# Optimization experiments

Hardware: AMD Instinct MI355X
Metric: run time of the kernel (lower is better)

The kernel has to match this reference:

```python
import jax, jax.numpy as jnp
import numpy as np

DIM_HEAD = 64
LN_EPS = 1e-6  # flax nn.LayerNorm default


def setup_inputs() -> dict:
    key = jax.random.key(0)
    ks = jax.random.split(key, 5)
    B, N, D, H, Dh = 4, 1024, 768, 12, 64
    x = jax.random.normal(ks[0], (B, N, D), dtype=jnp.float32)
    Wq = jax.random.normal(ks[1], (D, H, Dh), dtype=jnp.float32) * (1.0 / np.sqrt(D))
    Wk = jax.random.normal(ks[2], (D, H, Dh), dtype=jnp.float32) * (1.0 / np.sqrt(D))
    Wv = jax.random.normal(ks[3], (D, H, Dh), dtype=jnp.float32) * (1.0 / np.sqrt(D))
    theta = jax.random.normal(ks[4], (H, H), dtype=jnp.float32) * (1.0 / np.sqrt(H))
    ln_scale = jnp.ones((N,), dtype=jnp.float32)
    ln_bias = jnp.zeros((N,), dtype=jnp.float32)
    return {"x": x, "Wq": Wq, "Wk": Wk, "Wv": Wv, "theta": theta,
            "ln_scale": ln_scale, "ln_bias": ln_bias}


def reference(x, Wq, Wk, Wv, theta, ln_scale, ln_bias):
    # x: [B, N, D]; W*: [D, H, Dh]; theta: [H, H]; ln_*: [N]
    q = jnp.einsum('bnd,dhe->bnhe', x, Wq) / jnp.sqrt(jnp.float32(DIM_HEAD))
    k = jnp.einsum('bnd,dhe->bnhe', x, Wk)
    v = jnp.einsum('bnd,dhe->bnhe', x, Wv)
    # attention scores over key axis: [B, H, N, N]
    attn = jnp.einsum('bqhd,bkhd->bhqk', q, k)
    attn = jax.nn.softmax(attn, axis=-1)
    # cross-head theta mixing: 'h i, b h q k -> b i q k'
    attn = jnp.einsum('hi,bhqk->biqk', theta, attn)
    # LayerNorm over last (key) axis with learnable scale/bias of shape [N]
    mean = jnp.mean(attn, axis=-1, keepdims=True)
    var = jnp.mean(jnp.square(attn - mean), axis=-1, keepdims=True)
    attn = (attn - mean) * jax.lax.rsqrt(var + LN_EPS) * ln_scale + ln_bias
    # note: output indexed by k (as in the original source einsum)
    out = jnp.einsum('bhqk,bqhd->bkhd', attn, v)
    B, N, H, Dh = out.shape
    return out.reshape(B, N, H * Dh)
```

## Files before the change

kernel.cpp:

```cpp
#include <hip/hip_runtime.h>

#define NB    4
#define NSEQ  1024
#define DMODEL 768
#define NH    12
#define DH    64

typedef __bf16 bf16x8 __attribute__((ext_vector_type(8)));
typedef float  floatx4 __attribute__((ext_vector_type(4)));
typedef unsigned int u32;

static __device__ __forceinline__ float bf2f(unsigned short u) {
    return __uint_as_float(((unsigned)u) << 16);
}
static __device__ __forceinline__ unsigned short f2bf(float f) {
    unsigned u = __float_as_uint(f);
    u += 0x7FFFu + ((u >> 16) & 1u);
    return (unsigned short)(u >> 16);
}

static __device__ __forceinline__ void gl_lds16(const void* g, void* l) {
    __builtin_amdgcn_global_load_lds(
        (const __attribute__((address_space(1))) unsigned int*)g,
        (__attribute__((address_space(3))) unsigned int*)l, 16, 0, 0);
}

__global__ __launch_bounds__(256) void cast_x(
    const float* __restrict__ x, unsigned short* __restrict__ xb)
{
    const int g = blockIdx.x * 256 + threadIdx.x;
    const size_t base = (size_t)g * 8;
    float4 a = *(const float4*)(x + base);
    float4 b = *(const float4*)(x + base + 4);
    unsigned short o[8];
    o[0] = f2bf(a.x); o[1] = f2bf(a.y); o[2] = f2bf(a.z); o[3] = f2bf(a.w);
    o[4] = f2bf(b.x); o[5] = f2bf(b.y); o[6] = f2bf(b.z); o[7] = f2bf(b.w);
    *(uint4*)(xb + base) = *(uint4*)o;
}

__global__ __launch_bounds__(256) void tr_w(
    const float* __restrict__ Wq, const float* __restrict__ Wk,
    const float* __restrict__ Wv, unsigned short* __restrict__ Wt)
{
    const int z  = blockIdx.z;
    const float* __restrict__ W = (z == 0) ? Wq : (z == 1) ? Wk : Wv;
    const int c0 = blockIdx.x * 64;
    const int k0 = blockIdx.y * 64;
    const int t  = threadIdx.x;

    __shared__ float ls[64][65];

    const int lr = t >> 2;
    #pragma unroll
    for (int j = 0; j < 4; j++) {
        int col = (t & 3) * 16 + j * 4;
        float4 v = *(const float4*)(W + (size_t)(k0 + lr) * DMODEL + c0 + col);
        ls[lr][col + 0] = v.x; ls[lr][col + 1] = v.y;
        ls[lr][col + 2] = v.z; ls[lr][col + 3] = v.w;
    }
    __syncthreads();
    const int lc = t >> 2;
    #pragma unroll
    for (int j = 0; j < 4; j++) {
        int kb = (t & 3) * 16 + j * 4;
        ushort4 o;
        o.x = f2bf(ls[kb + 0][lc]); o.y = f2bf(ls[kb + 1][lc]);
        o.z = f2bf(ls[kb + 2][lc]); o.w = f2bf(ls[kb + 3][lc]);
        *(ushort4*)(Wt + (size_t)z * DMODEL * DMODEL + (size_t)(c0 + lc) * DMODEL + k0 + kb) = o;
    }
}

__global__ __launch_bounds__(256) void qkv_mfma(
    const unsigned short* __restrict__ xb, const unsigned short* __restrict__ Wt,
    unsigned short* __restrict__ Q, unsigned short* __restrict__ K,
    unsigned short* __restrict__ V)
{
    const int z  = blockIdx.z;
    const int r0 = blockIdx.x * 64;
    const int c0 = blockIdx.y * 128;
    const int t    = threadIdx.x;
    const int wave = t >> 6, lane = t & 63;
    const int m = lane & 15, g = lane >> 4;

    const unsigned short* __restrict__ B = Wt + (size_t)z * DMODEL * DMODEL;

    __shared__ __align__(16) char sm[17408];
    unsigned short (*As)[32] = (unsigned short(*)[32])sm;
    unsigned short (*Bs)[32] = (unsigned short(*)[32])(sm + 4096);
    unsigned short (*Po)[136] = (unsigned short(*)[136])sm;

    const int wm = (wave >> 1) * 32;
    const int wn = (wave & 1) * 64;

    floatx4 acc[2][4] = {};

    const unsigned short* ga  = xb + (size_t)(r0 + (t >> 2)) * DMODEL + (t & 3) * 8;
    const unsigned short* gb0 = B  + (size_t)(c0 + (t >> 2)) * DMODEL + (t & 3) * 8;
    const unsigned short* gb1 = B  + (size_t)(c0 + 64 + (t >> 2)) * DMODEL + (t & 3) * 8;
    unsigned short* la  = (unsigned short*)sm + (size_t)t * 8;
    unsigned short* lb0 = (unsigned short*)(sm + 4096) + (size_t)t * 8;
    unsigned short* lb1 = (unsigned short*)(sm + 4096) + (size_t)(t + 256) * 8;

    for (int kk = 0; kk < DMODEL / 32; kk++) {
        gl_lds16(ga  + kk * 32, la);
        gl_lds16(gb0 + kk * 32, lb0);
        gl_lds16(gb1 + kk * 32, lb1);
        __syncthreads();

        bf16x8 af[2], bf[4];
        #pragma unroll
        for (int mt = 0; mt < 2; mt++)
            af[mt] = *(const bf16x8*)&As[wm + mt * 16 + m][g * 8];
        #pragma unroll
        for (int nt = 0; nt < 4; nt++)
            bf[nt] = *(const bf16x8*)&Bs[wn + nt * 16 + m][g * 8];
        #pragma unroll
        for (int mt = 0; mt < 2; mt++)
            #pragma unroll
            for (int nt = 0; nt < 4; nt++)
                acc[mt][nt] = __builtin_amdgcn_mfma_f32_16x16x32_bf16(
                    af[mt], bf[nt], acc[mt][nt], 0, 0, 0);
        __syncthreads();
    }

    const float scale = (z == 0) ? 0.125f : 1.0f;
    #pragma unroll
    for (int mt = 0; mt < 2; mt++) {
        #pragma unroll
        for (int nt = 0; nt < 4; nt++) {
            int rloc = wm + mt * 16 + g * 4;
            int cloc = wn + nt * 16 + m;
            #pragma unroll
            for (int r = 0; r < 4; r++)
                Po[rloc + r][cloc] = f2bf(acc[mt][nt][r] * scale);
        }
    }
    __syncthreads();

    #pragma unroll
    for (int i = 0; i < 4; i++) {
        int ci = t + i * 256;
        int row = ci >> 4, off = (ci & 15) * 8;
        uint4 val = *(uint4*)&Po[row][off];
        if (z == 0) {
            *(uint4*)(Q + (size_t)(r0 + row) * DMODEL + c0 + off) = val;
        } else {
            unsigned short* P = (z == 1) ? K : V;
            int rr = r0 + row;
            int b = rr >> 10, n = rr & 1023;
            int cc = c0 + off;
            int h = cc >> 6, d = cc & 63;
            *(uint4*)(P + (((size_t)b * NH + h) * NSEQ + n) * DH + d) = val;
        }
    }
}

__global__ __launch_bounds__(256) void score_gemm(
    const unsigned short* __restrict__ Q, const unsigned short* __restrict__ K,
    unsigned short* __restrict__ P, float* __restrict__ Lpart)
{
    const int bh = blockIdx.z;
    const int b  = bh / NH, h = bh % NH;
    const int q0 = blockIdx.x * 128;
    const int k0 = blockIdx.y * 128;
    const int t    = threadIdx.x;
    const int wave = t >> 6, lane = t & 63;

    __shared__ __align__(16) char sm[36864];
    unsigned short (*Qs)[72] = (unsigned short(*)[72])sm;
    unsigned short (*Ks)[72] = (unsigned short(*)[72])(sm + 18432);
    unsigned short (*Po)[136] = (unsigned short(*)[136])sm;
    float (*rsum)[2] = (float(*)[2])(sm + 34816);

    #pragma unroll
    for (int i = 0; i < 4; i++) {
        int c = t + i * 256;
        int row = c >> 3, off = (c & 7) * 8;
        uint4 qa = *(const uint4*)(Q + ((size_t)(b * NSEQ + q0 + row)) * DMODEL + h * DH + off);
        uint4 ka = *(const uint4*)(K + (((size_t)bh) * NSEQ + (k0 + row)) * DH + off);
        *(uint4*)&Qs[row][off] = qa;
        *(uint4*)&Ks[row][off] = ka;
    }
    __syncthreads();

    const int wq = (wave >> 1) * 64, wk2 = (wave & 1) * 64;
    const int m = lane & 15, g = lane >> 4;

    floatx4 acc[4][4] = {};
    #pragma unroll
    for (int ds = 0; ds < 2; ds++) {
        const int dd = ds * 32 + g * 8;
        bf16x8 af[4], bf[4];
        #pragma unroll
        for (int mt = 0; mt < 4; mt++)
            af[mt] = *(const bf16x8*)&Qs[wq + mt * 16 + m][dd];
        #pragma unroll
        for (int nt = 0; nt < 4; nt++)
            bf[nt] = *(const bf16x8*)&Ks[wk2 + nt * 16 + m][dd];
        #pragma unroll
        for (int mt = 0; mt < 4; mt++)
            #pragma unroll
            for (int nt = 0; nt < 4; nt++)
                acc[mt][nt] = __builtin_amdgcn_mfma_f32_16x16x32_bf16(
                    af[mt], bf[nt], acc[mt][nt], 0, 0, 0);
    }

    __syncthreads();
    float rs[4][4] = {};
    #pragma unroll
    for (int mt = 0; mt < 4; mt++) {
        #pragma unroll
        for (int nt = 0; nt < 4; nt++) {
            int qloc = wq + mt * 16 + g * 4;
            int kloc = wk2 + nt * 16 + m;
            #pragma unroll
            for (int r = 0; r < 4; r++) {
                float e = __expf(acc[mt][nt][r]);
                Po[qloc + r][kloc] = f2bf(e);
                rs[mt][r] += e;
            }
        }
    }
    #pragma unroll
    for (int mt = 0; mt < 4; mt++)
        #pragma unroll
        for (int r = 0; r < 4; r++) {
            float x = rs[mt][r];
            #pragma unroll
            for (int off = 1; off < 16; off <<= 1)
                x += __shfl_xor(x, off, 64);
            rs[mt][r] = x;
        }
    if (m == 0) {
        #pragma unroll
        for (int mt = 0; mt < 4; mt++)
            #pragma unroll
            for (int r = 0; r < 4; r++)
                rsum[wq + mt * 16 + g * 4 + r][wk2 >> 6] = rs[mt][r];
    }
    __syncthreads();

    if (t < 128)
        Lpart[((size_t)bh * 8 + blockIdx.y) * NSEQ + q0 + t] = rsum[t][0] + rsum[t][1];

    #pragma unroll
    for (int i = 0; i < 8; i++) {
        int c = t + i * 256;
        int row = c >> 4, off = (c & 15) * 8;
        *(uint4*)(P + (((size_t)bh * NSEQ) + q0 + row) * NSEQ + k0 + off) =
            *(uint4*)&Po[row][off];
    }
}

static __device__ __forceinline__ void reduce12(
    const float* v, float* out12, float* red, int t)
{
    const int lane = t & 63, w = t >> 6;
    #pragma unroll
    for (int h = 0; h < 12; h++) {
        float x = v[h];
        #pragma unroll
        for (int off = 32; off > 0; off >>= 1)
            x += __shfl_down(x, off, 64);
        if (lane == 0) red[w * 12 + h] = x;
    }
    __syncthreads();
    if (t < 12) {
        float x = red[t];
        #pragma unroll
        for (int w2 = 1; w2 < 4; w2++) x += red[w2 * 12 + t];
        out12[t] = x;
    }
    __syncthreads();
}

__global__ __launch_bounds__(256) void mix_fused(
    unsigned short* __restrict__ P, const float* __restrict__ theta,
    const float* __restrict__ Lpart,
    const float* __restrict__ ln_scale, const float* __restrict__ ln_bias)
{
    const int q = blockIdx.x, b = blockIdx.y, t = threadIdx.x;
    __shared__ float th_s[144], red[48], l_s2[12], l_mean[12], l_rstd[12];

    if (t < 12) {
        float s = 0.f;
        #pragma unroll
        for (int kt = 0; kt < 8; kt++)
            s += Lpart[(((size_t)(b * NH + t)) * 8 + kt) * NSEQ + q];
        red[36 + t] = s;
        float mean = 0.f;
        #pragma unroll
        for (int h = 0; h < 12; h++) mean += theta[h * 12 + t];
        l_mean[t] = mean * (1.0f / 1024.0f);
    }
    __syncthreads();
    if (t < 144) th_s[t] = theta[t] * (1.0f / red[36 + t / 12]);
    __syncthreads();

    unsigned short* Pq = P + ((size_t)b * NH * NSEQ + q) * NSEQ;
    const int k0 = 4 * t;

    float p[12][4];
    #pragma unroll
    for (int h = 0; h < NH; h++) {
        ushort4 u = *(const ushort4*)(Pq + (size_t)h * NSEQ * NSEQ + k0);
        p[h][0] = bf2f(u.x); p[h][1] = bf2f(u.y);
        p[h][2] = bf2f(u.z); p[h][3] = bf2f(u.w);
    }

    float sT2[12];
    #pragma unroll
    for (int i = 0; i < 12; i++) {
        float s0 = 0.f, s1 = 0.f, s2 = 0.f, s3 = 0.f;
        #pragma unroll
        for (int h = 0; h < 12; h++) {
            float th = th_s[h * 12 + i];
            s0 = fmaf(th, p[h][0], s0); s1 = fmaf(th, p[h][1], s1);
            s2 = fmaf(th, p[h][2], s2); s3 = fmaf(th, p[h][3], s3);
        }
        sT2[i] = fmaf(s0, s0, fmaf(s1, s1, fmaf(s2, s2, s3 * s3)));
    }
    reduce12(sT2, l_s2, red, t);
    if (t < 12) {
        float mean = l_mean[t];
        float var  = l_s2[t] * (1.0f / 1024.0f) - mean * mean;
        l_rstd[t] = rsqrtf(var + 1e-6f);
    }
    __syncthreads();

    float4 lsc = *(const float4*)(ln_scale + k0);
    float4 lbs = *(const float4*)(ln_bias + k0);
    #pragma unroll
    for (int i = 0; i < 12; i++) {
        float s0 = 0.f, s1 = 0.f, s2 = 0.f, s3 = 0.f;
        #pragma unroll
        for (int h = 0; h < 12; h++) {
            float th = th_s[h * 12 + i];
            s0 = fmaf(th, p[h][0], s0); s1 = fmaf(th, p[h][1], s1);
            s2 = fmaf(th, p[h][2], s2); s3 = fmaf(th, p[h][3], s3);
        }
        float mm = l_mean[i], rs = l_rstd[i];
        ushort4 o;
        o.x = f2bf(fmaf((s0 - mm) * rs, lsc.x, lbs.x));
        o.y = f2bf(fmaf((s1 - mm) * rs, lsc.y, lbs.y));
        o.z = f2bf(fmaf((s2 - mm) * rs, lsc.z, lbs.z));
        o.w = f2bf(fmaf((s3 - mm) * rs, lsc.w, lbs.w));
        *(ushort4*)(Pq + (size_t)i * NSEQ * NSEQ + k0) = o;
    }
}

__global__ __launch_bounds__(256) void av_mfma(
    const unsigned short* __restrict__ A, const unsigned short* __restrict__ V,
    float* __restrict__ out)
{
    const int b  = blockIdx.z;
    const int i  = blockIdx.y;
    const int k0 = blockIdx.x * 64;
    const int t  = threadIdx.x;
    const int wave = t >> 6, lane = t & 63;
    const int m = lane & 15, g = lane >> 4;

    __shared__ __align__(16) u32 At[64 * 33];
    __shared__ __align__(16) u32 Vt[64 * 33];

    const unsigned short* Ai = A + ((size_t)(b * NH + i)) * NSEQ * NSEQ;
    const unsigned short* Vi = V + ((size_t)(b * NH + i)) * NSEQ * DH;

    const int wk = (wave >> 1) * 32;
    const int wd = (wave & 1) * 32;

    floatx4 acc[2][2] = {};

    for (int q0 = 0; q0 < NSEQ; q0 += 64) {
        ushort4 a0[2], a1[2], v0[2], v1[2];
        #pragma unroll
        for (int l = 0; l < 2; l++) {
            int c = t + l * 256;
            int k4 = (c & 15) * 4;
            int qp = c >> 4;
            a0[l] = *(const ushort4*)(Ai + (size_t)(q0 + 2 * qp)     * NSEQ + k0 + k4);
            a1[l] = *(const ushort4*)(Ai + (size_t)(q0 + 2 * qp + 1) * NSEQ + k0 + k4);
            v0[l] = *(const ushort4*)(Vi + (size_t)(q0 + 2 * qp)     * DH + k4);
            v1[l] = *(const ushort4*)(Vi + (size_t)(q0 + 2 * qp + 1) * DH + k4);
        }
        __syncthreads();
        #pragma unroll
        for (int l = 0; l < 2; l++) {
            int c = t + l * 256;
            int k4 = (c & 15) * 4;
            int qp = c >> 4;
            const unsigned short* pa0 = (const unsigned short*)&a0[l];
            const unsigned short* pa1 = (const unsigned short*)&a1[l];
            const unsigned short* pv0 = (const unsigned short*)&v0[l];
            const unsigned short* pv1 = (const unsigned short*)&v1[l];
            #pragma unroll
            for (int j = 0; j < 4; j++) {
                At[(k4 + j) * 33 + qp] = (u32)pa0[j] | ((u32)pa1[j] << 16);
                Vt[(k4 + j) * 33 + qp] = (u32)pv0[j] | ((u32)pv1[j] << 16);
            }
        }
        __syncthreads();

        #pragma unroll
        for (int ks = 0; ks < 2; ks++) {
            const int qo = ks * 16 + g * 4;
            bf16x8 af[2], bf[2];
            #pragma unroll
            for (int mt = 0; mt < 2; mt++) {
                const u32* r = &At[(wk + mt * 16 + m) * 33 + qo];
                uint4 w; w.x = r[0]; w.y = r[1]; w.z = r[2]; w.w = r[3];
                af[mt] = *(bf16x8*)&w;
            }
            #pragma unroll
            for (int nt = 0; nt < 2; nt++) {
                const u32* r = &Vt[(wd + nt * 16 + m) * 33 + qo];
                uint4 w; w.x = r[0]; w.y = r[1]; w.z = r[2]; w.w = r[3];
                bf[nt] = *(bf16x8*)&w;
            }
            #pragma unroll
            for (int mt = 0; mt < 2; mt++)
                #pragma unroll
                for (int nt = 0; nt < 2; nt++)
                    acc[mt][nt] = __builtin_amdgcn_mfma_f32_16x16x32_bf16(
                        af[mt], bf[nt], acc[mt][nt], 0, 0, 0);
        }
    }

    #pragma unroll
    for (int mt = 0; mt < 2; mt++) {
        #pragma unroll
        for (int nt = 0; nt < 2; nt++) {
            #pragma unroll
            for (int r = 0; r < 4; r++) {
                int k = k0 + wk + mt * 16 + g * 4 + r;
                int d = wd + nt * 16 + m;
                out[((size_t)(b * NSEQ + k)) * DMODEL + i * DH + d] = acc[mt][nt][r];
            }
        }
    }
}

extern "C" void kernel_launch(void* const* d_in, const int* in_sizes, int n_in,
                              void* d_out, int out_size, void* d_ws, size_t ws_size,
                              hipStream_t stream) {
    const float* x     = (const float*)d_in[0];
    const float* Wq    = (const float*)d_in[1];
    const float* Wk    = (const float*)d_in[2];
    const float* Wv    = (const float*)d_in[3];
    const float* theta = (const float*)d_in[4];
    const float* ln_s  = (const float*)d_in[5];
    const float* ln_b  = (const float*)d_in[6];
    float* out = (float*)d_out;

    char* ws = (char*)d_ws;
    const size_t qsz = (size_t)NB * NSEQ * DMODEL * sizeof(unsigned short);
    unsigned short* Q = (unsigned short*)(ws);
    unsigned short* K = (unsigned short*)(ws + qsz);
    unsigned short* V = (unsigned short*)(ws + 2 * qsz);
    unsigned short* P = (unsigned short*)(ws + 3 * qsz);
    unsigned short* xb = P;
    unsigned short* Wt = P + (size_t)NB * NSEQ * DMODEL;

    float* Lpart = out;

    cast_x<<<dim3(NB * NSEQ * DMODEL / 2048), 256, 0, stream>>>(x, xb);
    tr_w<<<dim3(12, 12, 3), 256, 0, stream>>>(Wq, Wk, Wv, Wt);
    qkv_mfma<<<dim3(NB * NSEQ / 64, DMODEL / 128, 3), 256, 0, stream>>>(
        xb, Wt, Q, K, V);
    score_gemm<<<dim3(NSEQ / 128, NSEQ / 128, NB * NH), 256, 0, stream>>>(Q, K, P, Lpart);
    mix_fused<<<dim3(NSEQ, NB), 256, 0, stream>>>(P, theta, Lpart, ln_s, ln_b);
    av_mfma<<<dim3(NSEQ / 64, NH, NB), 256, 0, stream>>>(P, V, out);
}
```

Baseline: 236.0 us.

## Fold LayerNorm normalization into AV GEMM via algebraic rescaling of V

The mix kernel now writes the un-normalized theta-mixed scores directly and stores only the per-row rstd in a side buffer, which removes the second 12x12 mixing pass. The AV kernel scales V rows by rstd while staging them and accumulates column sums of scaled and unscaled V. The mean and ln_scale/ln_bias terms are then applied as an epilogue correction. This trades recomputation in the mix kernel for extra conversion work in AV staging, and rounding the scaled V to bf16 may change numerical error.

```diff
diff --git a/kernel.cpp b/kernel.cpp
--- a/kernel.cpp
+++ b/kernel.cpp
@@ -274,13 +274,12 @@
     __syncthreads();
 }
 
-__global__ __launch_bounds__(256) void mix_fused(
+__global__ __launch_bounds__(256) void mix_t(
     unsigned short* __restrict__ P, const float* __restrict__ theta,
-    const float* __restrict__ Lpart,
-    const float* __restrict__ ln_scale, const float* __restrict__ ln_bias)
+    const float* __restrict__ Lpart, float* __restrict__ Rbuf)
 {
     const int q = blockIdx.x, b = blockIdx.y, t = threadIdx.x;
-    __shared__ float th_s[144], red[48], l_s2[12], l_mean[12], l_rstd[12];
+    __shared__ float th_s[144], red[48], l_s2[12], l_mean[12];
 
     if (t < 12) {
         float s = 0.f;
@@ -318,39 +317,23 @@
             s0 = fmaf(th, p[h][0], s0); s1 = fmaf(th, p[h][1], s1);
             s2 = fmaf(th, p[h][2], s2); s3 = fmaf(th, p[h][3], s3);
         }
+        ushort4 o;
+        o.x = f2bf(s0); o.y = f2bf(s1); o.z = f2bf(s2); o.w = f2bf(s3);
+        *(ushort4*)(Pq + (size_t)i * NSEQ * NSEQ + k0) = o;
         sT2[i] = fmaf(s0, s0, fmaf(s1, s1, fmaf(s2, s2, s3 * s3)));
     }
     reduce12(sT2, l_s2, red, t);
     if (t < 12) {
         float mean = l_mean[t];
         float var  = l_s2[t] * (1.0f / 1024.0f) - mean * mean;
-        l_rstd[t] = rsqrtf(var + 1e-6f);
-    }
-    __syncthreads();
-
-    float4 lsc = *(const float4*)(ln_scale + k0);
-    float4 lbs = *(const float4*)(ln_bias + k0);
-    #pragma unroll
-    for (int i = 0; i < 12; i++) {
-        float s0 = 0.f, s1 = 0.f, s2 = 0.f, s3 = 0.f;
-        #pragma unroll
-        for (int h = 0; h < 12; h++) {
-            float th = th_s[h * 12 + i];
-            s0 = fmaf(th, p[h][0], s0); s1 = fmaf(th, p[h][1], s1);
-            s2 = fmaf(th, p[h][2], s2); s3 = fmaf(th, p[h][3], s3);
-        }
-        float mm = l_mean[i], rs = l_rstd[i];
-        ushort4 o;
-        o.x = f2bf(fmaf((s0 - mm) * rs, lsc.x, lbs.x));
-        o.y = f2bf(fmaf((s1 - mm) * rs, lsc.y, lbs.y));
-        o.z = f2bf(fmaf((s2 - mm) * rs, lsc.z, lbs.z));
-        o.w = f2bf(fmaf((s3 - mm) * rs, lsc.w, lbs.w));
-        *(ushort4*)(Pq + (size_t)i * NSEQ * NSEQ + k0) = o;
+        Rbuf[(b * NH + t) * NSEQ + q] = rsqrtf(var + 1e-6f);
     }
 }
 
 __global__ __launch_bounds__(256) void av_mfma(
     const unsigned short* __restrict__ A, const unsigned short* __restrict__ V,
+    const float* __restrict__ Rbuf, const float* __restrict__ theta,
+    const float* __restrict__ ln_scale, const float* __restrict__ ln_bias,
     float* __restrict__ out)
 {
     const int b  = blockIdx.z;
@@ -360,19 +343,23 @@
     const int wave = t >> 6, lane = t & 63;
     const int m = lane & 15, g = lane >> 4;
 
-    __shared__ __align__(16) u32 At[64 * 33];
-    __shared__ __align__(16) u32 Vt[64 * 33];
+    __shared__ __align__(16) u32 At[64 * 33 + 64];
+    __shared__ __align__(16) u32 Vt[64 * 33 + 64];
 
     const unsigned short* Ai = A + ((size_t)(b * NH + i)) * NSEQ * NSEQ;
     const unsigned short* Vi = V + ((size_t)(b * NH + i)) * NSEQ * DH;
+    const float* Rb = Rbuf + (size_t)(b * NH + i) * NSEQ;
 
     const int wk = (wave >> 1) * 32;
     const int wd = (wave & 1) * 32;
 
     floatx4 acc[2][2] = {};
+    float c1[4] = {}, c2[4] = {};
+    const int k4s = (t & 15) * 4;
 
     for (int q0 = 0; q0 < NSEQ; q0 += 64) {
         ushort4 a0[2], a1[2], v0[2], v1[2];
+        float2 rr[2];
         #pragma unroll
         for (int l = 0; l < 2; l++) {
             int c = t + l * 256;
@@ -382,6 +369,7 @@
             a1[l] = *(const ushort4*)(Ai + (size_t)(q0 + 2 * qp + 1) * NSEQ + k0 + k4);
             v0[l] = *(const ushort4*)(Vi + (size_t)(q0 + 2 * qp)     * DH + k4);
             v1[l] = *(const ushort4*)(Vi + (size_t)(q0 + 2 * qp + 1) * DH + k4);
+            rr[l] = *(const float2*)(Rb + q0 + 2 * qp);
         }
         __syncthreads();
         #pragma unroll
@@ -396,7 +384,11 @@
             #pragma unroll
             for (int j = 0; j < 4; j++) {
                 At[(k4 + j) * 33 + qp] = (u32)pa0[j] | ((u32)pa1[j] << 16);
-                Vt[(k4 + j) * 33 + qp] = (u32)pv0[j] | ((u32)pv1[j] << 16);
+                float vf0 = bf2f(pv0[j]), vf1 = bf2f(pv1[j]);
+                float s0 = rr[l].x * vf0, s1 = rr[l].y * vf1;
+                Vt[(k4 + j) * 33 + qp] = (u32)f2bf(s0) | ((u32)f2bf(s1) << 16);
+                c1[j] += s0 + s1;
+                c2[j] += vf0 + vf1;
             }
         }
         __syncthreads();
@@ -426,15 +418,47 @@
         }
     }
 
+    __syncthreads();
+    float* c1l = (float*)At;
+    float* c2l = (float*)Vt;
+    const int grp = t >> 4;
+    #pragma unroll
+    for (int j = 0; j < 4; j++) {
+        c1l[grp * 64 + k4s + j] = c1[j];
+        c2l[grp * 64 + k4s + j] = c2[j];
+    }
+    __syncthreads();
+    if (t < 64) {
+        float s1_ = 0.f, s2_ = 0.f;
+        #pragma unroll
+        for (int g2 = 0; g2 < 16; g2++) {
+            s1_ += c1l[g2 * 64 + t];
+            s2_ += c2l[g2 * 64 + t];
+        }
+        c1l[1024 + t] = s1_;
+        c2l[1024 + t] = s2_;
+    }
+    __syncthreads();
+
+    float mean = 0.f;
+    #pragma unroll
+    for (int h = 0; h < 12; h++) mean += theta[h * 12 + i];
+    mean *= (1.0f / 1024.0f);
+
     #pragma unroll
     for (int mt = 0; mt < 2; mt++) {
+        int kb = k0 + wk + mt * 16 + g * 4;
+        float4 ls4 = *(const float4*)(ln_scale + kb);
+        float4 lb4 = *(const float4*)(ln_bias + kb);
         #pragma unroll
         for (int nt = 0; nt < 2; nt++) {
+            int d = wd + nt * 16 + m;
+            float C1d = c1l[1024 + d], C2d = c2l[1024 + d];
             #pragma unroll
             for (int r = 0; r < 4; r++) {
-                int k = k0 + wk + mt * 16 + g * 4 + r;
-                int d = wd + nt * 16 + m;
-                out[((size_t)(b * NSEQ + k)) * DMODEL + i * DH + d] = acc[mt][nt][r];
+                float lns = (&ls4.x)[r], lnb = (&lb4.x)[r];
+                float val = lns * (acc[mt][nt][r] - mean * C1d) + lnb * C2d;
+                out[((size_t)(b * NSEQ + kb + r)) * DMODEL + i * DH + d] = val;
             }
         }
     }
@@ -462,12 +486,14 @@
     unsigned short* Wt = P + (size_t)NB * NSEQ * DMODEL;
 
     float* Lpart = out;
+    float* Rbuf  = (float*)K;
 
     cast_x<<<dim3(NB * NSEQ * DMODEL / 2048), 256, 0, stream>>>(x, xb);
     tr_w<<<dim3(12, 12, 3), 256, 0, stream>>>(Wq, Wk, Wv, Wt);
     qkv_mfma<<<dim3(NB * NSEQ / 64, DMODEL / 128, 3), 256, 0, stream>>>(
         xb, Wt, Q, K, V);
     score_gemm<<<dim3(NSEQ / 128, NSEQ / 128, NB * NH), 256, 0, stream>>>(Q, K, P, Lpart);
-    mix_fused<<<dim3(NSEQ, NB), 256, 0, stream>>>(P, theta, Lpart, ln_s, ln_b);
-    av_mfma<<<dim3(NSEQ / 64, NH, NB), 256, 0, stream>>>(P, V, out);
-}
+    mix_t<<<dim3(NSEQ, NB), 256, 0, stream>>>(P, theta, Lpart, Rbuf);
+    av_mfma<<<dim3(NSEQ / 64, NH, NB), 256, 0, stream>>>(
+        P, V, Rbuf, theta, ln_s, ln_b, out);
+}
```

New measurement: 216.3 us. 8.3% less time.
